# Kernel optimization log

Hardware: AMD Instinct MI355X
Metric: run time of the kernel (lower is better)

Reference implementation:

```python
import jax, jax.numpy as jnp
import numpy as np

NUM_HEADS = 8
HEAD_SIZE = 64
INPUT = 512
OUT = NUM_HEADS * HEAD_SIZE
B, S = 4, 2048


def setup_inputs() -> dict:
    key = jax.random.key(0)
    ks = jax.random.split(key, 6)
    return {
        "key": jax.random.normal(ks[0], (B, S, INPUT), dtype=jnp.float32),
        "key_mask": jnp.zeros((B, 1, 1, S), dtype=jnp.float32),
        "query": jax.random.normal(ks[1], (B, S, INPUT), dtype=jnp.float32),
        "value": jax.random.normal(ks[2], (B, S, INPUT), dtype=jnp.float32),
        "wq": jax.random.normal(ks[3], (INPUT, OUT), dtype=jnp.float32) * (INPUT ** -0.5),
        "wk": jax.random.normal(ks[4], (INPUT, OUT), dtype=jnp.float32) * (INPUT ** -0.5),
        "wv": jax.random.normal(ks[5], (INPUT, OUT), dtype=jnp.float32) * (INPUT ** -0.5),
    }


def _split_heads(x):
    # [B, S, H*hd] -> [B, H, S, hd]
    b, s, _ = x.shape
    return x.reshape(b, s, NUM_HEADS, HEAD_SIZE).transpose(0, 2, 1, 3)


def reference(key, key_mask, query, value, wq, wk, wv):
    q = _split_heads(query @ wq)   # [B,H,S,hd]
    k = _split_heads(key @ wk)
    v = _split_heads(value @ wv)
    scale = 1.0 / jnp.sqrt(jnp.asarray(HEAD_SIZE, q.dtype))
    logits = jnp.einsum('bhqd,bhkd->bhqk', q, k) * scale + key_mask
    attn = jax.nn.softmax(logits, axis=-1)
    out = jnp.einsum('bhqk,bhkd->bhqd', attn, v)  # [B,H,S,hd]
    out = out.transpose(0, 2, 1, 3).reshape(out.shape[0], out.shape[2], OUT)
    return out
```

## Files before the change

### kernel.cpp

```cpp
#include <hip/hip_runtime.h>

typedef _Float16 f16;
typedef f16 f16x8 __attribute__((ext_vector_type(8)));
typedef f16 f16x4 __attribute__((ext_vector_type(4)));
typedef f16 f16x2 __attribute__((ext_vector_type(2)));
typedef float f32x4 __attribute__((ext_vector_type(4)));
typedef float f32x16 __attribute__((ext_vector_type(16)));
typedef unsigned int u32;
typedef u32 u32x2 __attribute__((ext_vector_type(2)));
typedef u32 u32x4 __attribute__((ext_vector_type(4)));

#define MFMA16(a, b, c) __builtin_amdgcn_mfma_f32_16x16x32_f16(a, b, c, 0, 0, 0)
#define MFMA32(a, b, c) __builtin_amdgcn_mfma_f32_32x32x16_f16(a, b, c, 0, 0, 0)

#define BATCH 4
#define NHEADS 8
#define HDIM 64
#define SEQ 2048
#define DIN 512
#define DOUT 512
#define LOG2E 1.44269504f
#define C1 0.18033688f

__device__ __forceinline__ void gl_lds16(const void* g, const void* l) {
  __builtin_amdgcn_global_load_lds(
      (const __attribute__((address_space(1))) u32*)g,
      (__attribute__((address_space(3))) u32*)l, 16, 0, 0);
}

__device__ __forceinline__ float fexp2(float x) {
  float r;
  asm("v_exp_f32 %0, %1" : "=v"(r) : "v"(x));
  return r;
}

__device__ __forceinline__ u32 pk2u(float a, float b) {
  return __builtin_bit_cast(u32, __builtin_amdgcn_cvt_pkrtz(a, b));
}

__device__ __forceinline__ f16x2 pk2(float a, float b) {
  return __builtin_bit_cast(f16x2, __builtin_amdgcn_cvt_pkrtz(a, b));
}

__device__ __forceinline__ f16x4 pk4(float a, float b, float c, float d) {
  f16x2 u0 = pk2(a, b), u1 = pk2(c, d);
  f16x4 r;
  r[0] = u0[0]; r[1] = u0[1]; r[2] = u1[0]; r[3] = u1[1];
  return r;
}

__global__ __launch_bounds__(256) void prep_w(
    const float* __restrict__ wq, const float* __restrict__ wk,
    const float* __restrict__ wv, f16* __restrict__ wT) {
  __shared__ float tile[64][65];
  const float* w = blockIdx.z == 0 ? wq : (blockIdx.z == 1 ? wk : wv);
  f16* out = wT + (size_t)blockIdx.z * DIN * DOUT;
  int k0 = blockIdx.x * 64, n0 = blockIdx.y * 64;
  int t = threadIdx.x;
  int c = t & 63, rb = t >> 6;
#pragma unroll
  for (int ph = 0; ph < 16; ++ph) {
    int r = ph * 4 + rb;
    tile[r][c] = w[(size_t)(k0 + r) * DOUT + n0 + c];
  }
  __syncthreads();
#pragma unroll
  for (int ph = 0; ph < 16; ++ph) {
    int n = ph * 4 + rb;
    out[(size_t)(n0 + n) * DIN + k0 + c] = (f16)tile[c][n];
  }
}

__global__ __launch_bounds__(256, 3) void qkv_gemm(
    const float* __restrict__ xq, const float* __restrict__ xk,
    const float* __restrict__ xv, const f16* __restrict__ wT,
    f16* __restrict__ Qo, f16* __restrict__ Ko, f16* __restrict__ Vt) {
  __shared__ __attribute__((aligned(16))) f16 smem[16384];
  f16* As = smem;
  f16* Bs = smem + 8192;
  f16* CT = smem;

  int gemm = blockIdx.z;
  const float* x = gemm == 0 ? xq : (gemm == 1 ? xk : xv);
  const f16* wt = wT + (size_t)gemm * DIN * DOUT;
  int bx = blockIdx.x;
  int m0 = (bx & 63) * 128, n0 = (bx >> 6) * 128;
  int t = threadIdx.x, w = t >> 6, lane = t & 63;
  int lr = lane & 15, lq = lane >> 4;
  int wm = (w >> 1) * 64, wn = (w & 1) * 64;

  int tr = t >> 4, tc = t & 15;
  const float* xg = x + (size_t)(m0 + tr) * DIN + tc * 4;
  int aw[8];
#pragma unroll
  for (int ph = 0; ph < 8; ++ph) {
    int r = tr + 16 * ph;
    int phys = (tc >> 1) ^ (r & 7);
    aw[ph] = r * 64 + phys * 8 + (tc & 1) * 4;
  }

  int srow = lane >> 3;
  int schunk = (lane & 7) ^ srow;
  const f16* gb[4];
  const f16* lbb[4];
#pragma unroll
  for (int j = 0; j < 4; ++j) {
    int br = w * 32 + j * 8;
    gb[j] = wt + (size_t)(n0 + br + srow) * DIN + schunk * 8;
    lbb[j] = &Bs[__builtin_amdgcn_readfirstlane(br * 64)];
  }
  int xo0 = ((0 * 4 + lq) ^ (lr & 7)) * 8;
  int xo1 = ((1 * 4 + lq) ^ (lr & 7)) * 8;

  f32x4 zero = {0.f, 0.f, 0.f, 0.f};
  f32x4 acc[4][4];
#pragma unroll
  for (int i = 0; i < 4; ++i)
#pragma unroll
    for (int j = 0; j < 4; ++j) acc[i][j] = zero;

  for (int k0 = 0; k0 < DIN; k0 += 64) {
    __syncthreads();
#pragma unroll
    for (int j = 0; j < 4; ++j) gl_lds16(gb[j] + k0, lbb[j]);
#pragma unroll
    for (int ph = 0; ph < 8; ++ph) {
      float4 a = *(const float4*)(xg + (size_t)ph * 16 * DIN + k0);
      *(f16x4*)&As[aw[ph]] = pk4(a.x, a.y, a.z, a.w);
    }
    __syncthreads();
#pragma unroll
    for (int c = 0; c < 2; ++c) {
      int xo = c ? xo1 : xo0;
      f16x8 xf[4], wf[4];
#pragma unroll
      for (int i = 0; i < 4; ++i)
        xf[i] = *(const f16x8*)&As[(wm + i * 16 + lr) * 64 + xo];
#pragma unroll
      for (int i = 0; i < 4; ++i)
        wf[i] = *(const f16x8*)&Bs[(wn + i * 16 + lr) * 64 + xo];
      if (gemm == 2) {
#pragma unroll
        for (int i = 0; i < 4; ++i)
#pragma unroll
          for (int j = 0; j < 4; ++j)
            acc[i][j] = MFMA16(xf[i], wf[j], acc[i][j]);
      } else {
#pragma unroll
        for (int i = 0; i < 4; ++i)
#pragma unroll
          for (int j = 0; j < 4; ++j)
            acc[i][j] = MFMA16(wf[i], xf[j], acc[i][j]);
      }
    }
  }

  __syncthreads();
  int b_ = m0 >> 11;
  int sl = m0 & 2047;

  if (gemm == 2) {
#pragma unroll
    for (int i = 0; i < 4; ++i) {
#pragma unroll
      for (int j = 0; j < 4; ++j) {
        int d = wn + j * 16 + lr;
        int lc = (wm >> 3) + i * 2 + (lq >> 1);
        int phys = lc ^ lr;
        *(f16x4*)&CT[d * 128 + phys * 8 + (lq & 1) * 4] =
            pk4(acc[i][j][0], acc[i][j][1], acc[i][j][2], acc[i][j][3]);
      }
    }
    __syncthreads();
    int tid16 = t & 15;
#pragma unroll
    for (int ph = 0; ph < 8; ++ph) {
      int d = ph * 16 + (t >> 4);
      int phys = tid16 ^ (d & 15);
      f16x8 vv = *(const f16x8*)&CT[d * 128 + phys * 8];
      int hgl = (n0 + d) >> 6, dd = (n0 + d) & 63;
      *(f16x8*)&Vt[(((size_t)b_ * NHEADS + hgl) * HDIM + dd) * SEQ + sl +
                   tid16 * 8] = vv;
    }
  } else {
    f16* O = gemm == 0 ? Qo : Ko;
    float sc = gemm == 0 ? C1 : 1.0f;
#pragma unroll
    for (int i = 0; i < 4; ++i) {
#pragma unroll
      for (int j = 0; j < 4; ++j) {
        int s = wm + j * 16 + lr;
        int lc = (wn >> 3) + i * 2 + (lq >> 1);
        int phys = lc ^ lr;
        *(f16x4*)&CT[s * 128 + phys * 8 + (lq & 1) * 4] =
            pk4(acc[i][j][0] * sc, acc[i][j][1] * sc, acc[i][j][2] * sc,
                acc[i][j][3] * sc);
      }
    }
    __syncthreads();
    int tid8 = t & 7;
    int hh = (t >> 3) & 1;
#pragma unroll
    for (int ph = 0; ph < 8; ++ph) {
      int s = ph * 16 + (t >> 4);
      int lc = hh * 8 + tid8;
      int phys = lc ^ (s & 15);
      f16x8 vv = *(const f16x8*)&CT[s * 128 + phys * 8];
      int hgl = (n0 >> 6) + hh;
      *(f16x8*)&O[(((size_t)b_ * NHEADS + hgl) * SEQ + sl + s) * HDIM +
                  tid8 * 8] = vv;
    }
  }
}

__global__ __launch_bounds__(256, 2) void flash_attn(
    const f16* __restrict__ Q, const f16* __restrict__ K,
    const f16* __restrict__ Vt, const float* __restrict__ mask,
    float* __restrict__ out) {
  __shared__ __attribute__((aligned(16))) f16 Ks[2 * 128 * 64];
  __shared__ __attribute__((aligned(16))) f16 Vs[2 * 64 * 128];
  __shared__ __attribute__((aligned(16))) float Ms[SEQ];

  int bh = blockIdx.x, q0 = blockIdx.y * 128;
  int b = bh >> 3, h = bh & 7;
  int t = threadIdx.x, w = t >> 6, lane = t & 63;
  int lr = lane & 15, lq = lane >> 4;
  int l5 = lane & 31, hf = lane >> 5;

  const f16* Qg = Q + (size_t)bh * SEQ * HDIM;
  const f16* Kg = K + (size_t)bh * SEQ * HDIM;
  const f16* Vg = Vt + (size_t)bh * HDIM * SEQ;
  const float* mg = mask + (size_t)b * SEQ;

  int krow = lane >> 3;
  int kchunk = (lane & 7) ^ krow;
  const f16* gk[4];
  const f16* gv[4];
  const f16* lk[4];
  const f16* lv[4];
#pragma unroll
  for (int j = 0; j < 4; ++j) {
    int kbr = w * 32 + j * 8;
    gk[j] = Kg + (size_t)(kbr + krow) * HDIM + kchunk * 8;
    lk[j] = &Ks[__builtin_amdgcn_readfirstlane(kbr * 64)];
    int vbr = w * 16 + j * 4;
    int vchunk = (lane & 15) ^ ((vbr + lq) & 15);
    gv[j] = Vg + (size_t)(vbr + lq) * SEQ + vchunk * 8;
    lv[j] = &Vs[__builtin_amdgcn_readfirstlane(vbr * 128)];
  }

  {
    int c0 = w * 512;
    gl_lds16(mg + c0 + lane * 4, &Ms[__builtin_amdgcn_readfirstlane(c0)]);
    gl_lds16(mg + c0 + 256 + lane * 4,
             &Ms[__builtin_amdgcn_readfirstlane(c0 + 256)]);
  }
#pragma unroll
  for (int j = 0; j < 4; ++j) {
    gl_lds16(gk[j], lk[j]);
    gl_lds16(gv[j], lv[j]);
  }

  f16x8 qf[4];
#pragma unroll
  for (int ds = 0; ds < 4; ++ds)
    qf[ds] = *(const f16x8*)(Qg + (size_t)(q0 + w * 32 + l5) * HDIM + ds * 16 +
                             hf * 8);

  f32x16 acc[2];
#pragma unroll
  for (int dt = 0; dt < 2; ++dt)
#pragma unroll
    for (int i = 0; i < 16; ++i) acc[dt][i] = 0.f;
  float lsum = 0.f;

  asm volatile("s_waitcnt vmcnt(0)" ::: "memory");
  __builtin_amdgcn_sched_barrier(0);
  __builtin_amdgcn_s_barrier();
  __builtin_amdgcn_sched_barrier(0);

  for (int it = 0; it < 16; ++it) {
    int p = it & 1;
    int k0 = it * 128;
    const f16* Kb = &Ks[p * 8192];
    const f16* Vb = &Vs[p * 8192];

    if (it < 15) {
      int pn = p ^ 1;
#pragma unroll
      for (int j = 0; j < 4; ++j) {
        gl_lds16(gk[j] + (size_t)(k0 + 128) * HDIM, lk[j] + pn * 8192);
        gl_lds16(gv[j] + k0 + 128, lv[j] + pn * 8192);
      }
    }

    u32 pk_[4][4][2];

#pragma unroll
    for (int nt = 0; nt < 4; ++nt) {
      f32x16 s = {0.f, 0.f, 0.f, 0.f, 0.f, 0.f, 0.f, 0.f,
                  0.f, 0.f, 0.f, 0.f, 0.f, 0.f, 0.f, 0.f};
      __builtin_amdgcn_s_setprio(1);
#pragma unroll
      for (int ds = 0; ds < 4; ++ds) {
        f16x8 kf = *(const f16x8*)&Kb[(nt * 32 + l5) * 64 +
                                      (((ds * 2 + hf) ^ (l5 & 7)) * 8)];
        s = MFMA32(kf, qf[ds], s);
      }
      __builtin_amdgcn_s_setprio(0);
#pragma unroll
      for (int run = 0; run < 4; ++run) {
        float4 mk = *(const float4*)&Ms[k0 + nt * 32 + run * 8 + 4 * hf];
        float p0 = fexp2(fmaf(mk.x, LOG2E, s[run * 4 + 0]));
        float p1 = fexp2(fmaf(mk.y, LOG2E, s[run * 4 + 1]));
        float p2 = fexp2(fmaf(mk.z, LOG2E, s[run * 4 + 2]));
        float p3 = fexp2(fmaf(mk.w, LOG2E, s[run * 4 + 3]));
        lsum += (p0 + p1) + (p2 + p3);
        pk_[nt][run][0] = pk2u(p0, p1);
        pk_[nt][run][1] = pk2u(p2, p3);
      }
    }

    __builtin_amdgcn_s_setprio(1);
#pragma unroll
    for (int ks = 0; ks < 8; ++ks) {
      const int nt = ks >> 1;
      const int ge = 2 * (ks & 1);
      const int go = 2 * (ks & 1) + 1;
      u32x2 r0 = __builtin_amdgcn_permlane32_swap(pk_[nt][ge][0],
                                                  pk_[nt][go][0], false, false);
      u32x2 r1 = __builtin_amdgcn_permlane32_swap(pk_[nt][ge][1],
                                                  pk_[nt][go][1], false, false);
      u32x4 apw = {r0[0], r1[0], r0[1], r1[1]};
      f16x8 ap = __builtin_bit_cast(f16x8, apw);
#pragma unroll
      for (int dt = 0; dt < 2; ++dt) {
        f16x8 bv = *(const f16x8*)&Vb[(dt * 32 + l5) * 128 +
                                      (((ks * 2 + hf) ^ (l5 & 15)) * 8)];
        acc[dt] = MFMA32(ap, bv, acc[dt]);
      }
    }
    __builtin_amdgcn_s_setprio(0);

    asm volatile("s_waitcnt vmcnt(0)" ::: "memory");
    __builtin_amdgcn_sched_barrier(0);
    __builtin_amdgcn_s_barrier();
    __builtin_amdgcn_sched_barrier(0);
  }

  float l = lsum + __shfl_xor(lsum, 32);
  float inv = 1.f / l;
  Ms[w * 32 + l5] = inv;
  asm volatile("s_waitcnt lgkmcnt(0)" ::: "memory");
  __builtin_amdgcn_sched_barrier(0);
  float ivq[16];
#pragma unroll
  for (int r = 0; r < 16; ++r)
    ivq[r] = Ms[w * 32 + (r & 3) + 8 * (r >> 2) + 4 * hf];

#pragma unroll
  for (int dt = 0; dt < 2; ++dt) {
#pragma unroll
    for (int r = 0; r < 16; ++r) {
      int q = q0 + w * 32 + (r & 3) + 8 * (r >> 2) + 4 * hf;
      int d = h * HDIM + dt * 32 + l5;
      out[((size_t)b * SEQ + q) * DOUT + d] = acc[dt][r] * ivq[r];
    }
  }
}

extern "C" void kernel_launch(void* const* d_in, const int* in_sizes, int n_in,
                              void* d_out, int out_size, void* d_ws,
                              size_t ws_size, hipStream_t stream) {
  const float* key = (const float*)d_in[0];
  const float* key_mask = (const float*)d_in[1];
  const float* query = (const float*)d_in[2];
  const float* value = (const float*)d_in[3];
  const float* wq = (const float*)d_in[4];
  const float* wk = (const float*)d_in[5];
  const float* wv = (const float*)d_in[6];
  float* out = (float*)d_out;

  char* ws = (char*)d_ws;
  f16* Qws = (f16*)(ws);
  f16* Kws = (f16*)(ws + 8388608);
  f16* Vtws = (f16*)(ws + 16777216);
  f16* wT = (f16*)(ws + 25165824);

  prep_w<<<dim3(8, 8, 3), 256, 0, stream>>>(wq, wk, wv, wT);
  qkv_gemm<<<dim3(256, 1, 3), 256, 0, stream>>>(query, key, value, wT, Qws,
                                                Kws, Vtws);
  flash_attn<<<dim3(32, 16), 256, 0, stream>>>(Qws, Kws, Vtws, key_mask, out);
}
```

Before: 180.1 us.

## Interleave QK^T MFMAs with softmax exp and compute row sums via MFMA

```diff
diff --git a/kernel.cpp b/kernel.cpp
--- a/kernel.cpp
+++ b/kernel.cpp
@@ -224,7 +224,6 @@
   int bh = blockIdx.x, q0 = blockIdx.y * 128;
   int b = bh >> 3, h = bh & 7;
   int t = threadIdx.x, w = t >> 6, lane = t & 63;
-  int lr = lane & 15, lq = lane >> 4;
   int l5 = lane & 31, hf = lane >> 5;
 
   const f16* Qg = Q + (size_t)bh * SEQ * HDIM;
@@ -244,6 +243,7 @@
     gk[j] = Kg + (size_t)(kbr + krow) * HDIM + kchunk * 8;
     lk[j] = &Ks[__builtin_amdgcn_readfirstlane(kbr * 64)];
     int vbr = w * 16 + j * 4;
+    int lq = lane >> 4;
     int vchunk = (lane & 15) ^ ((vbr + lq) & 15);
     gv[j] = Vg + (size_t)(vbr + lq) * SEQ + vchunk * 8;
     lv[j] = &Vs[__builtin_amdgcn_readfirstlane(vbr * 128)];
@@ -267,17 +267,45 @@
     qf[ds] = *(const f16x8*)(Qg + (size_t)(q0 + w * 32 + l5) * HDIM + ds * 16 +
                              hf * 8);
 
+  u32x4 ow = {0x3C003C00u, 0x3C003C00u, 0x3C003C00u, 0x3C003C00u};
+  f16x8 ones = __builtin_bit_cast(f16x8, ow);
+
+  const f32x16 Z = {0.f, 0.f, 0.f, 0.f, 0.f, 0.f, 0.f, 0.f,
+                    0.f, 0.f, 0.f, 0.f, 0.f, 0.f, 0.f, 0.f};
   f32x16 acc[2];
-#pragma unroll
-  for (int dt = 0; dt < 2; ++dt)
-#pragma unroll
-    for (int i = 0; i < 16; ++i) acc[dt][i] = 0.f;
-  float lsum = 0.f;
+  f32x16 acc_l = Z;
+#pragma unroll
+  for (int dt = 0; dt < 2; ++dt) acc[dt] = Z;
 
   asm volatile("s_waitcnt vmcnt(0)" ::: "memory");
   __builtin_amdgcn_sched_barrier(0);
   __builtin_amdgcn_s_barrier();
   __builtin_amdgcn_sched_barrier(0);
+
+#define QKT(nt, sv)                                                          \
+  {                                                                          \
+    __builtin_amdgcn_s_setprio(1);                                           \
+    f16x8 kf0 = *(const f16x8*)&Kb[((nt)*32 + l5) * 64 +                     \
+                                   (((0 + hf) ^ (l5 & 7)) * 8)];             \
+    sv = MFMA32(kf0, qf[0], Z);                                              \
+    _Pragma("unroll") for (int ds = 1; ds < 4; ++ds) {                       \
+      f16x8 kf = *(const f16x8*)&Kb[((nt)*32 + l5) * 64 +                    \
+                                    (((ds * 2 + hf) ^ (l5 & 7)) * 8)];       \
+      sv = MFMA32(kf, qf[ds], sv);                                           \
+    }                                                                        \
+    __builtin_amdgcn_s_setprio(0);                                           \
+  }
+
+#define SM(nt, sv)                                                           \
+  _Pragma("unroll") for (int run = 0; run < 4; ++run) {                      \
+    float4 mk = *(const float4*)&Ms[k0 + (nt)*32 + run * 8 + 4 * hf];        \
+    float p0 = fexp2(fmaf(mk.x, LOG2E, sv[run * 4 + 0]));                    \
+    float p1 = fexp2(fmaf(mk.y, LOG2E, sv[run * 4 + 1]));                    \
+    float p2 = fexp2(fmaf(mk.z, LOG2E, sv[run * 4 + 2]));                    \
+    float p3 = fexp2(fmaf(mk.w, LOG2E, sv[run * 4 + 3]));                    \
+    pk_[nt][run][0] = pk2u(p0, p1);                                          \
+    pk_[nt][run][1] = pk2u(p2, p3);                                          \
+  }
 
   for (int it = 0; it < 16; ++it) {
     int p = it & 1;
@@ -296,29 +324,16 @@
 
     u32 pk_[4][4][2];
 
-#pragma unroll
-    for (int nt = 0; nt < 4; ++nt) {
-      f32x16 s = {0.f, 0.f, 0.f, 0.f, 0.f, 0.f, 0.f, 0.f,
-                  0.f, 0.f, 0.f, 0.f, 0.f, 0.f, 0.f, 0.f};
-      __builtin_amdgcn_s_setprio(1);
-#pragma unroll
-      for (int ds = 0; ds < 4; ++ds) {
-        f16x8 kf = *(const f16x8*)&Kb[(nt * 32 + l5) * 64 +
-                                      (((ds * 2 + hf) ^ (l5 & 7)) * 8)];
-        s = MFMA32(kf, qf[ds], s);
-      }
-      __builtin_amdgcn_s_setprio(0);
-#pragma unroll
-      for (int run = 0; run < 4; ++run) {
-        float4 mk = *(const float4*)&Ms[k0 + nt * 32 + run * 8 + 4 * hf];
-        float p0 = fexp2(fmaf(mk.x, LOG2E, s[run * 4 + 0]));
-        float p1 = fexp2(fmaf(mk.y, LOG2E, s[run * 4 + 1]));
-        float p2 = fexp2(fmaf(mk.z, LOG2E, s[run * 4 + 2]));
-        float p3 = fexp2(fmaf(mk.w, LOG2E, s[run * 4 + 3]));
-        lsum += (p0 + p1) + (p2 + p3);
-        pk_[nt][run][0] = pk2u(p0, p1);
-        pk_[nt][run][1] = pk2u(p2, p3);
-      }
+    {
+      f32x16 sA, sB;
+      QKT(0, sA);
+      QKT(1, sB);
+      SM(0, sA);
+      QKT(2, sA);
+      SM(1, sB);
+      QKT(3, sB);
+      SM(2, sA);
+      SM(3, sB);
     }
 
     __builtin_amdgcn_s_setprio(1);
@@ -333,6 +348,7 @@
                                                   pk_[nt][go][1], false, false);
       u32x4 apw = {r0[0], r1[0], r0[1], r1[1]};
       f16x8 ap = __builtin_bit_cast(f16x8, apw);
+      acc_l = MFMA32(ap, ones, acc_l);
 #pragma unroll
       for (int dt = 0; dt < 2; ++dt) {
         f16x8 bv = *(const f16x8*)&Vb[(dt * 32 + l5) * 128 +
@@ -347,16 +363,12 @@
     __builtin_amdgcn_s_barrier();
     __builtin_amdgcn_sched_barrier(0);
   }
-
-  float l = lsum + __shfl_xor(lsum, 32);
-  float inv = 1.f / l;
-  Ms[w * 32 + l5] = inv;
-  asm volatile("s_waitcnt lgkmcnt(0)" ::: "memory");
-  __builtin_amdgcn_sched_barrier(0);
+#undef QKT
+#undef SM
+
   float ivq[16];
 #pragma unroll
-  for (int r = 0; r < 16; ++r)
-    ivq[r] = Ms[w * 32 + (r & 3) + 8 * (r >> 2) + 4 * hf];
+  for (int r = 0; r < 16; ++r) ivq[r] = 1.f / acc_l[r];
 
 #pragma unroll
   for (int dt = 0; dt < 2; ++dt) {
```

Result: no change. 181.7 us (+0.9%).
